# Performance work log

Hardware: AMD Instinct MI355X
Metric: run time of the kernel (lower is better)

The kernel has to match this reference:

```python
import jax, jax.numpy as jnp
import numpy as np

N_NODES = 100000
N_EDGES = 3200000
N_FEAT = 512
NHID = 256
LATENT = 64

def _spmm(edge_index, edge_weight, h, num_nodes):
    # out[dst] = sum_e w_e * h[src_e]  (sparse adj @ h)
    src, dst = edge_index[0], edge_index[1]
    msgs = edge_weight[:, None] * h[src]            # [E, D]
    return jax.ops.segment_sum(msgs, dst, num_segments=num_nodes)

def _gcn_conv(x, edge_index, edge_weight, W, b, num_nodes):
    # GCNConv: adj @ (x @ W) + b
    return _spmm(edge_index, edge_weight, x @ W, num_nodes) + b

def setup_inputs() -> dict:
    key = jax.random.key(0)
    ks = jax.random.split(key, 8)
    x = jax.random.normal(ks[0], (N_NODES, N_FEAT), dtype=jnp.float32)
    edge_index = jax.random.randint(ks[1], (2, N_EDGES), 0, N_NODES, dtype=jnp.int32)
    edge_weight = jax.random.uniform(ks[2], (N_EDGES,), dtype=jnp.float32)
    s1 = 1.0 / np.sqrt(N_FEAT)
    s2 = 1.0 / np.sqrt(NHID)
    W1 = jax.random.normal(ks[3], (N_FEAT, NHID), dtype=jnp.float32) * s1
    b1 = jnp.zeros((NHID,), dtype=jnp.float32)
    W_mu = jax.random.normal(ks[4], (NHID, LATENT), dtype=jnp.float32) * s2
    b_mu = jnp.zeros((LATENT,), dtype=jnp.float32)
    W_logvar = jax.random.normal(ks[5], (NHID, LATENT), dtype=jnp.float32) * s2
    b_logvar = jnp.zeros((LATENT,), dtype=jnp.float32)
    return {"x": x, "edge_index": edge_index, "edge_weight": edge_weight,
            "W1": W1, "b1": b1, "W_mu": W_mu, "b_mu": b_mu,
            "W_logvar": W_logvar, "b_logvar": b_logvar}

def reference(x, edge_index, edge_weight, W1, b1, W_mu, b_mu, W_logvar, b_logvar):
    n = x.shape[0]
    # dropout is identity in eval mode (training=False)
    h = jax.nn.relu(_gcn_conv(x, edge_index, edge_weight, W1, b1, n))  # [N, nhid]
    mu = _gcn_conv(h, edge_index, edge_weight, W_mu, b_mu, n)          # [N, latent]
    logvar = _gcn_conv(h, edge_index, edge_weight, W_logvar, b_logvar, n)
    return (mu, logvar)
```

## Files before the change

### kernel.cpp

```cpp
#include <hip/hip_runtime.h>
#include <hip/hip_bf16.h>

#define NN 100000
#define NE 3200000
#define NF 512
#define NH 256
#define NL 64
#define PAD 40

#define NBKT 250
#define NPB 400
#define CAP 13600
#define EPB 12800

typedef __bf16 bf16x8 __attribute__((ext_vector_type(8)));
typedef __bf16 bf16x4 __attribute__((ext_vector_type(4)));
typedef __bf16 bf16x2 __attribute__((ext_vector_type(2)));
typedef float  f32x4  __attribute__((ext_vector_type(4)));

__global__ void k_prep(const float* __restrict__ W1, const float* __restrict__ Wmu,
                       const float* __restrict__ Wlv, __bf16* __restrict__ P1,
                       __bf16* __restrict__ P2, int* __restrict__ bcur) {
    int bid = blockIdx.x;
    int tid = threadIdx.x;
    if (bid < 512) {
        int i = bid * 256 + tid;
        int j = i & 7, l = (i >> 3) & 63, kc = (i >> 9) & 15, nt = i >> 13;
        int k = kc * 32 + (l >> 4) * 8 + j;
        int n = nt * 16 + (l & 15);
        P1[i] = (__bf16)W1[k * NH + n];
    } else if (bid < 640) {
        int i = (bid - 512) * 256 + tid;
        int j = i & 7, l = (i >> 3) & 63, kc = (i >> 9) & 7, nt = i >> 12;
        int k = kc * 32 + (l >> 4) * 8 + j;
        int n = nt * 16 + (l & 15);
        float v = (n < NL) ? Wmu[k * NL + n] : Wlv[k * NL + (n - NL)];
        P2[i] = (__bf16)v;
    } else {
        if (tid < NBKT) bcur[tid * 16] = tid * CAP;
    }
}

__global__ __launch_bounds__(256) void k_bucket0(const int* __restrict__ src,
                                                 const int* __restrict__ dst,
                                                 const int* __restrict__ wbits,
                                                 int* __restrict__ bcur,
                                                 int2* __restrict__ stage) {
    __shared__ int cnt[NBKT];
    __shared__ int cur[NBKT];
    int tid = threadIdx.x;
    int e0 = blockIdx.x * EPB;
    if (tid < NBKT) cnt[tid] = 0;
    __syncthreads();
    for (int k = 0; k < EPB / 256; k++) {
        int d = dst[e0 + k * 256 + tid];
        atomicAdd(&cnt[(unsigned)d / NPB], 1);
    }
    __syncthreads();
    if (tid < NBKT) cur[tid] = atomicAdd(&bcur[tid * 16], cnt[tid]);
    __syncthreads();
    for (int k = 0; k < EPB / 256; k++) {
        int e = e0 + k * 256 + tid;
        int d = dst[e];
        int b = (int)((unsigned)d / NPB);
        int pos = atomicAdd(&cur[b], 1);
        stage[pos] = make_int2(src[e] | ((d - b * NPB) << 17), wbits[e]);
    }
}

__global__ void k_bscan(const int* __restrict__ bcur, int* __restrict__ bstart) {
    __shared__ int s[256];
    int t = threadIdx.x;
    int v = (t < NBKT) ? (bcur[t * 16] - t * CAP) : 0;
    s[t] = v;
    __syncthreads();
    for (int off = 1; off < 256; off <<= 1) {
        int a = (t >= off) ? s[t - off] : 0;
        __syncthreads();
        s[t] += a;
        __syncthreads();
    }
    if (t < NBKT) bstart[t] = s[t] - v;
}

__global__ __launch_bounds__(512) void k_build(const int2* __restrict__ stage,
                                               const int* __restrict__ bcur,
                                               const int* __restrict__ bstart,
                                               int* __restrict__ deg,
                                               int* __restrict__ row_ptr,
                                               int2* __restrict__ sedge) {
    __shared__ int hist[NPB];
    __shared__ int sb[2][512];
    int b = blockIdx.x;
    int t = threadIdx.x;
    int n0 = b * NPB;
    int s0 = b * CAP;
    int fill = bcur[b * 16] - s0;

    if (t < NPB) hist[t] = 0;
    __syncthreads();
    for (int i = t; i < fill; i += 512)
        atomicAdd(&hist[(unsigned)stage[s0 + i].x >> 17], 1);
    __syncthreads();
    int v = (t < NPB) ? hist[t] : 0;
    int buf = 0;
    sb[0][t] = v;
    __syncthreads();
    for (int off = 1; off < 512; off <<= 1) {
        int nv = sb[buf][t] + ((t >= off) ? sb[buf][t - off] : 0);
        buf ^= 1;
        sb[buf][t] = nv;
        __syncthreads();
    }
    int base = bstart[b];
    if (t < NPB) {
        int abs0 = base + sb[buf][t] - v;
        deg[n0 + t] = v;
        row_ptr[n0 + t] = abs0;
        hist[t] = abs0;
    }
    __syncthreads();
    for (int i = t; i < fill; i += 512) {
        int2 sv = stage[s0 + i];
        int dl = (unsigned)sv.x >> 17;
        int pos = atomicAdd(&hist[dl], 1);
        sedge[pos] = make_int2(sv.x & 0x1FFFF, sv.y);
    }
}

__global__ __launch_bounds__(256) void k_gemm1(const float* __restrict__ x,
                                               const __bf16* __restrict__ Wp,
                                               __bf16* __restrict__ T) {
    __shared__ __bf16 As[64 * PAD];
    int tid = threadIdx.x;
    int wv = tid >> 6, lane = tid & 63;
    int quad = lane >> 4, l16 = lane & 15;
    long m0 = (long)blockIdx.x * 64;

    int srow = tid >> 2;
    int scol = (tid & 3) * 8;
    long grow = m0 + srow; if (grow > NN - 1) grow = NN - 1;
    const float* xrow = x + grow * NF;

    f32x4 acc[4][4];
#pragma unroll
    for (int a = 0; a < 4; a++)
#pragma unroll
        for (int b = 0; b < 4; b++) acc[a][b] = (f32x4)0.f;

    float4 p0 = *(const float4*)(xrow + scol);
    float4 p1 = *(const float4*)(xrow + scol + 4);

    for (int kc = 0; kc < 16; kc++) {
        union { bf16x8 v; __bf16 e[8]; } u;
        u.e[0] = (__bf16)p0.x; u.e[1] = (__bf16)p0.y;
        u.e[2] = (__bf16)p0.z; u.e[3] = (__bf16)p0.w;
        u.e[4] = (__bf16)p1.x; u.e[5] = (__bf16)p1.y;
        u.e[6] = (__bf16)p1.z; u.e[7] = (__bf16)p1.w;
        *(bf16x8*)&As[srow * PAD + scol] = u.v;
        __syncthreads();
        if (kc < 15) {
            p0 = *(const float4*)(xrow + (kc + 1) * 32 + scol);
            p1 = *(const float4*)(xrow + (kc + 1) * 32 + scol + 4);
        }
        bf16x8 bfr[4];
#pragma unroll
        for (int nt = 0; nt < 4; nt++)
            bfr[nt] = *(const bf16x8*)(Wp + (((long)(wv * 4 + nt) * 16 + kc) * 64 + lane) * 8);
#pragma unroll
        for (int mt = 0; mt < 4; mt++) {
            bf16x8 af = *(const bf16x8*)&As[(mt * 16 + l16) * PAD + quad * 8];
#pragma unroll
            for (int nt = 0; nt < 4; nt++)
                acc[mt][nt] = __builtin_amdgcn_mfma_f32_16x16x32_bf16(af, bfr[nt], acc[mt][nt], 0, 0, 0);
        }
        __syncthreads();
    }
#pragma unroll
    for (int mt = 0; mt < 4; mt++)
#pragma unroll
        for (int r = 0; r < 4; r++) {
            long gr = m0 + mt * 16 + quad * 4 + r;
            if (gr < NN) {
#pragma unroll
                for (int nt = 0; nt < 4; nt++)
                    T[gr * 256 + wv * 64 + nt * 16 + l16] = (__bf16)acc[mt][nt][r];
            }
        }
}

__global__ __launch_bounds__(256) void k_spmm_h(const __bf16* __restrict__ T,
                                                const int2* __restrict__ sedge,
                                                const int* __restrict__ row_ptr,
                                                const int* __restrict__ deg,
                                                const float* __restrict__ bias,
                                                __bf16* __restrict__ o) {
    int wave = threadIdx.x >> 6, lane = threadIdx.x & 63;
    int n = blockIdx.x * 4 + wave;
    if (n >= NN) return;
    int i = row_ptr[n];
    int end = i + deg[n];
    float a0 = 0.f, a1 = 0.f, a2 = 0.f, a3 = 0.f;
    const bf16x4* base = (const bf16x4*)T;
    for (; i + 16 <= end; i += 16) {
        int2 e[16];
#pragma unroll
        for (int k = 0; k < 16; k++) e[k] = sedge[i + k];
        bf16x4 v[16];
#pragma unroll
        for (int k = 0; k < 16; k++) v[k] = base[(long)e[k].x * 64 + lane];
#pragma unroll
        for (int k = 0; k < 16; k++) {
            float w = __uint_as_float(e[k].y);
            a0 += w * (float)v[k][0];
            a1 += w * (float)v[k][1];
            a2 += w * (float)v[k][2];
            a3 += w * (float)v[k][3];
        }
    }
    for (; i + 4 <= end; i += 4) {
        int2 e[4];
#pragma unroll
        for (int k = 0; k < 4; k++) e[k] = sedge[i + k];
        bf16x4 v[4];
#pragma unroll
        for (int k = 0; k < 4; k++) v[k] = base[(long)e[k].x * 64 + lane];
#pragma unroll
        for (int k = 0; k < 4; k++) {
            float w = __uint_as_float(e[k].y);
            a0 += w * (float)v[k][0];
            a1 += w * (float)v[k][1];
            a2 += w * (float)v[k][2];
            a3 += w * (float)v[k][3];
        }
    }
    for (; i < end; i++) {
        int2 e = sedge[i];
        float w = __uint_as_float(e.y);
        bf16x4 v = base[(long)e.x * 64 + lane];
        a0 += w * (float)v[0]; a1 += w * (float)v[1];
        a2 += w * (float)v[2]; a3 += w * (float)v[3];
    }
    float4 bv = ((const float4*)bias)[lane];
    bf16x4 ov;
    ov[0] = (__bf16)fmaxf(a0 + bv.x, 0.f);
    ov[1] = (__bf16)fmaxf(a1 + bv.y, 0.f);
    ov[2] = (__bf16)fmaxf(a2 + bv.z, 0.f);
    ov[3] = (__bf16)fmaxf(a3 + bv.w, 0.f);
    ((bf16x4*)o)[(long)n * 64 + lane] = ov;
}

__global__ __launch_bounds__(256) void k_gemm2(const __bf16* __restrict__ h,
                                               const __bf16* __restrict__ Wp,
                                               __bf16* __restrict__ HMb) {
    __shared__ __bf16 As[128 * PAD];
    int tid = threadIdx.x;
    int wv = tid >> 6, lane = tid & 63;
    int quad = lane >> 4, l16 = lane & 15;
    int wr = (wv >> 1) * 64, wc = (wv & 1) * 64;
    long m0 = (long)blockIdx.x * 128;

    int srow = tid >> 1;
    int scol = (tid & 1) * 16;
    long grow = m0 + srow; if (grow > NN - 1) grow = NN - 1;

    f32x4 acc[4][4];
#pragma unroll
    for (int a = 0; a < 4; a++)
#pragma unroll
        for (int b = 0; b < 4; b++) acc[a][b] = (f32x4)0.f;

    const __bf16* rH = h + grow * 256;
    bf16x8 p0 = *(const bf16x8*)(rH + scol);
    bf16x8 p1 = *(const bf16x8*)(rH + scol + 8);

    for (int kc = 0; kc < 8; kc++) {
        *(bf16x8*)&As[srow * PAD + scol] = p0;
        *(bf16x8*)&As[srow * PAD + scol + 8] = p1;
        __syncthreads();
        if (kc < 7) {
            const __bf16* nxt = rH + (kc + 1) * 32;
            p0 = *(const bf16x8*)(nxt + scol);
            p1 = *(const bf16x8*)(nxt + scol + 8);
        }
        bf16x8 bfr[4];
#pragma unroll
        for (int nt = 0; nt < 4; nt++) {
            int ntg = (wc >> 4) + nt;
            bfr[nt] = *(const bf16x8*)(Wp + (((long)ntg * 8 + kc) * 64 + lane) * 8);
        }
#pragma unroll
        for (int mt = 0; mt < 4; mt++) {
            bf16x8 af = *(const bf16x8*)&As[(wr + mt * 16 + l16) * PAD + quad * 8];
#pragma unroll
            for (int nt = 0; nt < 4; nt++)
                acc[mt][nt] = __builtin_amdgcn_mfma_f32_16x16x32_bf16(af, bfr[nt], acc[mt][nt], 0, 0, 0);
        }
        __syncthreads();
    }
#pragma unroll
    for (int mt = 0; mt < 4; mt++)
#pragma unroll
        for (int r = 0; r < 4; r++) {
            long gr = m0 + wr + mt * 16 + quad * 4 + r;
            if (gr < NN) {
#pragma unroll
                for (int nt = 0; nt < 4; nt++)
                    HMb[gr * 128 + wc + nt * 16 + l16] = (__bf16)acc[mt][nt][r];
            }
        }
}

__global__ __launch_bounds__(256) void k_spmm2(const __bf16* __restrict__ HMb,
                                               const int2* __restrict__ sedge,
                                               const int* __restrict__ row_ptr,
                                               const int* __restrict__ deg,
                                               const float* __restrict__ bmu,
                                               const float* __restrict__ blv,
                                               float* __restrict__ out) {
    int wave = threadIdx.x >> 6, lane = threadIdx.x & 63;
    int n = blockIdx.x * 4 + wave;
    if (n >= NN) return;
    int i = row_ptr[n];
    int end = i + deg[n];
    float a0 = 0.f, a1 = 0.f;
    const bf16x2* base = (const bf16x2*)HMb;
    for (; i + 16 <= end; i += 16) {
        int2 e[16];
#pragma unroll
        for (int k = 0; k < 16; k++) e[k] = sedge[i + k];
        bf16x2 v[16];
#pragma unroll
        for (int k = 0; k < 16; k++) v[k] = base[(long)e[k].x * 64 + lane];
#pragma unroll
        for (int k = 0; k < 16; k++) {
            float w = __uint_as_float(e[k].y);
            a0 += w * (float)v[k][0];
            a1 += w * (float)v[k][1];
        }
    }
    for (; i + 4 <= end; i += 4) {
        int2 e[4];
#pragma unroll
        for (int k = 0; k < 4; k++) e[k] = sedge[i + k];
        bf16x2 v[4];
#pragma unroll
        for (int k = 0; k < 4; k++) v[k] = base[(long)e[k].x * 64 + lane];
#pragma unroll
        for (int k = 0; k < 4; k++) {
            float w = __uint_as_float(e[k].y);
            a0 += w * (float)v[k][0];
            a1 += w * (float)v[k][1];
        }
    }
    for (; i < end; i++) {
        int2 e = sedge[i];
        float w = __uint_as_float(e.y);
        bf16x2 v = base[(long)e.x * 64 + lane];
        a0 += w * (float)v[0]; a1 += w * (float)v[1];
    }
    if (lane < 32) {
        float2 b = ((const float2*)bmu)[lane];
        float2 o = {a0 + b.x, a1 + b.y};
        ((float2*)out)[(long)n * 32 + lane] = o;
    } else {
        float2 b = ((const float2*)blv)[lane - 32];
        float2 o = {a0 + b.x, a1 + b.y};
        ((float2*)(out + (long)NN * NL))[(long)n * 32 + (lane - 32)] = o;
    }
}

extern "C" void kernel_launch(void* const* d_in, const int* in_sizes, int n_in,
                              void* d_out, int out_size, void* d_ws, size_t ws_size,
                              hipStream_t stream) {
    const float* x   = (const float*)d_in[0];
    const int*   ei  = (const int*)d_in[1];
    const float* ew  = (const float*)d_in[2];
    const float* W1  = (const float*)d_in[3];
    const float* b1  = (const float*)d_in[4];
    const float* Wmu = (const float*)d_in[5];
    const float* bmu = (const float*)d_in[6];
    const float* Wlv = (const float*)d_in[7];
    const float* blv = (const float*)d_in[8];
    float* out = (float*)d_out;

    char* ws = (char*)d_ws;
    __bf16* XW     = (__bf16*)(ws);
    __bf16* h      = (__bf16*)(ws + 51200000);
    __bf16* HMb    = (__bf16*)(ws + 102400000);
    int2*  sedge   = (int2*) (ws + 128000000);
    int*   deg     = (int*)  (ws + 153600000);
    int*   row_ptr = (int*)  (ws + 154000000);
    int*   bcur    = (int*)  (ws + 154400000);
    int*   bstart  = (int*)  (ws + 154800000);
    __bf16* Wp1    = (__bf16*)(ws + 154900000);
    __bf16* Wp2    = (__bf16*)(ws + 155200000);

    int2* stage = (int2*)(ws + 51200000);

    const int* esrc = ei;
    const int* edst = ei + NE;

    k_prep<<<dim3(641), dim3(256), 0, stream>>>(W1, Wmu, Wlv, Wp1, Wp2, bcur);

    k_bucket0<<<dim3(NBKT), dim3(256), 0, stream>>>(esrc, edst, (const int*)ew,
                                                    bcur, stage);
    k_bscan<<<dim3(1), dim3(256), 0, stream>>>(bcur, bstart);
    k_build<<<dim3(NBKT), dim3(512), 0, stream>>>(stage, bcur, bstart,
                                                  deg, row_ptr, sedge);

    k_gemm1<<<dim3((NN + 63) / 64), dim3(256), 0, stream>>>(x, Wp1, XW);
    k_spmm_h<<<dim3((NN + 3) / 4), dim3(256), 0, stream>>>(XW, sedge, row_ptr, deg, b1, h);

    k_gemm2<<<dim3((NN + 127) / 128), dim3(256), 0, stream>>>(h, Wp2, HMb);
    k_spmm2<<<dim3((NN + 3) / 4), dim3(256), 0, stream>>>(HMb, sedge, row_ptr, deg, bmu, blv, out);
}
```

Baseline: 793.5 us.

## Co-schedule CSR build kernels with the first GEMM in combined launches

```diff
diff --git a/kernel.cpp b/kernel.cpp
--- a/kernel.cpp
+++ b/kernel.cpp
@@ -12,6 +12,8 @@
 #define NPB 400
 #define CAP 13600
 #define EPB 12800
+#define GA  781
+#define GB  782
 
 typedef __bf16 bf16x8 __attribute__((ext_vector_type(8)));
 typedef __bf16 bf16x4 __attribute__((ext_vector_type(4)));
@@ -41,13 +43,14 @@
     }
 }
 
-__global__ __launch_bounds__(256) void k_bucket0(const int* __restrict__ src,
-                                                 const int* __restrict__ dst,
-                                                 const int* __restrict__ wbits,
-                                                 int* __restrict__ bcur,
-                                                 int2* __restrict__ stage) {
-    __shared__ int cnt[NBKT];
-    __shared__ int cur[NBKT];
+__device__ __forceinline__ void bucket0_body(char* smem,
+                                             const int* __restrict__ src,
+                                             const int* __restrict__ dst,
+                                             const int* __restrict__ wbits,
+                                             int* __restrict__ bcur,
+                                             int2* __restrict__ stage) {
+    int* cnt = (int*)smem;
+    int* cur = cnt + NBKT;
     int tid = threadIdx.x;
     int e0 = blockIdx.x * EPB;
     if (tid < NBKT) cnt[tid] = 0;
@@ -68,59 +71,40 @@
     }
 }
 
-__global__ void k_bscan(const int* __restrict__ bcur, int* __restrict__ bstart) {
-    __shared__ int s[256];
-    int t = threadIdx.x;
-    int v = (t < NBKT) ? (bcur[t * 16] - t * CAP) : 0;
-    s[t] = v;
-    __syncthreads();
-    for (int off = 1; off < 256; off <<= 1) {
-        int a = (t >= off) ? s[t - off] : 0;
-        __syncthreads();
-        s[t] += a;
-        __syncthreads();
-    }
-    if (t < NBKT) bstart[t] = s[t] - v;
-}
-
-__global__ __launch_bounds__(512) void k_build(const int2* __restrict__ stage,
-                                               const int* __restrict__ bcur,
-                                               const int* __restrict__ bstart,
-                                               int* __restrict__ deg,
-                                               int* __restrict__ row_ptr,
-                                               int2* __restrict__ sedge) {
-    __shared__ int hist[NPB];
-    __shared__ int sb[2][512];
+__device__ __forceinline__ void build_body(char* smem,
+                                           const int2* __restrict__ stage,
+                                           const int* __restrict__ bcur,
+                                           const int* __restrict__ bstart,
+                                           int* __restrict__ deg,
+                                           int* __restrict__ row_ptr,
+                                           int2* __restrict__ sedge) {
+    int* hist = (int*)smem;
+    int* roff = hist + NPB;
     int b = blockIdx.x;
     int t = threadIdx.x;
     int n0 = b * NPB;
     int s0 = b * CAP;
     int fill = bcur[b * 16] - s0;
-
-    if (t < NPB) hist[t] = 0;
-    __syncthreads();
-    for (int i = t; i < fill; i += 512)
+    for (int i = t; i < NPB; i += 256) hist[i] = 0;
+    __syncthreads();
+    for (int i = t; i < fill; i += 256)
         atomicAdd(&hist[(unsigned)stage[s0 + i].x >> 17], 1);
     __syncthreads();
-    int v = (t < NPB) ? hist[t] : 0;
-    int buf = 0;
-    sb[0][t] = v;
-    __syncthreads();
-    for (int off = 1; off < 512; off <<= 1) {
-        int nv = sb[buf][t] + ((t >= off) ? sb[buf][t - off] : 0);
-        buf ^= 1;
-        sb[buf][t] = nv;
-        __syncthreads();
-    }
+    if (t == 0) {
+        int acc = 0;
+        for (int i = 0; i < NPB; i++) { roff[i] = acc; acc += hist[i]; }
+    }
+    __syncthreads();
     int base = bstart[b];
-    if (t < NPB) {
-        int abs0 = base + sb[buf][t] - v;
-        deg[n0 + t] = v;
-        row_ptr[n0 + t] = abs0;
-        hist[t] = abs0;
-    }
-    __syncthreads();
-    for (int i = t; i < fill; i += 512) {
+    for (int i = t; i < NPB; i += 256) {
+        int c = hist[i];
+        int a = base + roff[i];
+        deg[n0 + i] = c;
+        row_ptr[n0 + i] = a;
+        hist[i] = a;
+    }
+    __syncthreads();
+    for (int i = t; i < fill; i += 256) {
         int2 sv = stage[s0 + i];
         int dl = (unsigned)sv.x >> 17;
         int pos = atomicAdd(&hist[dl], 1);
@@ -128,14 +112,15 @@
     }
 }
 
-__global__ __launch_bounds__(256) void k_gemm1(const float* __restrict__ x,
-                                               const __bf16* __restrict__ Wp,
-                                               __bf16* __restrict__ T) {
-    __shared__ __bf16 As[64 * PAD];
+__device__ __forceinline__ void gemm1_body(char* smem, int mb,
+                                           const float* __restrict__ x,
+                                           const __bf16* __restrict__ Wp,
+                                           __bf16* __restrict__ T) {
+    __bf16* As = (__bf16*)smem;
     int tid = threadIdx.x;
     int wv = tid >> 6, lane = tid & 63;
     int quad = lane >> 4, l16 = lane & 15;
-    long m0 = (long)blockIdx.x * 64;
+    long m0 = (long)mb * 64;
 
     int srow = tid >> 2;
     int scol = (tid & 3) * 8;
@@ -187,6 +172,52 @@
                     T[gr * 256 + wv * 64 + nt * 16 + l16] = (__bf16)acc[mt][nt][r];
             }
         }
+}
+
+__global__ __launch_bounds__(256) void k_phase1(const int* __restrict__ src,
+                                                const int* __restrict__ dst,
+                                                const int* __restrict__ wbits,
+                                                int* __restrict__ bcur,
+                                                int2* __restrict__ stage,
+                                                const float* __restrict__ x,
+                                                const __bf16* __restrict__ Wp,
+                                                __bf16* __restrict__ T) {
+    __shared__ __align__(16) char smem[5120];
+    if (blockIdx.x < NBKT)
+        bucket0_body(smem, src, dst, wbits, bcur, stage);
+    else
+        gemm1_body(smem, blockIdx.x - NBKT, x, Wp, T);
+}
+
+__global__ __launch_bounds__(256) void k_phase2(const int2* __restrict__ stage,
+                                                const int* __restrict__ bcur,
+                                                const int* __restrict__ bstart,
+                                                int* __restrict__ deg,
+                                                int* __restrict__ row_ptr,
+                                                int2* __restrict__ sedge,
+                                                const float* __restrict__ x,
+                                                const __bf16* __restrict__ Wp,
+                                                __bf16* __restrict__ T) {
+    __shared__ __align__(16) char smem[5120];
+    if (blockIdx.x < NBKT)
+        build_body(smem, stage, bcur, bstart, deg, row_ptr, sedge);
+    else
+        gemm1_body(smem, blockIdx.x - NBKT + GA, x, Wp, T);
+}
+
+__global__ void k_bscan(const int* __restrict__ bcur, int* __restrict__ bstart) {
+    __shared__ int s[256];
+    int t = threadIdx.x;
+    int v = (t < NBKT) ? (bcur[t * 16] - t * CAP) : 0;
+    s[t] = v;
+    __syncthreads();
+    for (int off = 1; off < 256; off <<= 1) {
+        int a = (t >= off) ? s[t - off] : 0;
+        __syncthreads();
+        s[t] += a;
+        __syncthreads();
+    }
+    if (t < NBKT) bstart[t] = s[t] - v;
 }
 
 __global__ __launch_bounds__(256) void k_spmm_h(const __bf16* __restrict__ T,
@@ -403,13 +434,13 @@
 
     k_prep<<<dim3(641), dim3(256), 0, stream>>>(W1, Wmu, Wlv, Wp1, Wp2, bcur);
 
-    k_bucket0<<<dim3(NBKT), dim3(256), 0, stream>>>(esrc, edst, (const int*)ew,
-                                                    bcur, stage);
+    k_phase1<<<dim3(NBKT + GA), dim3(256), 0, stream>>>(esrc, edst, (const int*)ew,
+                                                        bcur, stage, x, Wp1, XW);
     k_bscan<<<dim3(1), dim3(256), 0, stream>>>(bcur, bstart);
-    k_build<<<dim3(NBKT), dim3(512), 0, stream>>>(stage, bcur, bstart,
-                                                  deg, row_ptr, sedge);
-
-    k_gemm1<<<dim3((NN + 63) / 64), dim3(256), 0, stream>>>(x, Wp1, XW);
+    k_phase2<<<dim3(NBKT + GB), dim3(256), 0, stream>>>(stage, bcur, bstart,
+                                                        deg, row_ptr, sedge,
+                                                        x, Wp1, XW);
+
     k_spmm_h<<<dim3((NN + 3) / 4), dim3(256), 0, stream>>>(XW, sedge, row_ptr, deg, b1, h);
 
     k_gemm2<<<dim3((NN + 127) / 128), dim3(256), 0, stream>>>(h, Wp2, HMb);
```

Result: faster. 777.4 us (-2.0%).
